# Performance work log

Hardware: AMD Instinct MI355X
Metric: run time of the kernel (lower is better)

Reference implementation:

```python
import jax, jax.numpy as jnp
import numpy as np
import math

N = 50000      # nodes
E = 800000     # edges
F_IN = 64      # input node features
H = 4          # heads
C = 32         # hidden_channels (per-head dim)
HC = H * C     # 128
ED = 4         # edge_dim
G = 1000       # graphs in batch


def _lin(key, fin, fout, bias=True):
    k1, k2 = jax.random.split(key)
    w = jax.random.normal(k1, (fin, fout), jnp.float32) * (1.0 / math.sqrt(fin))
    if bias:
        b = jax.random.normal(k2, (fout,), jnp.float32) * 0.02
        return w, b
    return w


def setup_inputs() -> dict:
    key = jax.random.key(0)
    ks = jax.random.split(key, 24)
    x = jax.random.normal(ks[0], (N, F_IN), jnp.float32)
    edge_index = jax.random.randint(ks[1], (2, E), 0, N)
    edge_attr = jax.random.normal(ks[2], (E, ED), jnp.float32)
    batch = jnp.sort(jax.random.randint(ks[3], (N,), 0, G))
    inp = {"x": x, "edge_index": edge_index, "edge_attr": edge_attr, "batch": batch}
    fins = [F_IN, HC, HC]
    i = 4
    for l in range(3):
        fin = fins[l]
        inp[f"wq{l+1}"], inp[f"bq{l+1}"] = _lin(ks[i], fin, HC); i += 1
        inp[f"wk{l+1}"], inp[f"bk{l+1}"] = _lin(ks[i], fin, HC); i += 1
        inp[f"wv{l+1}"], inp[f"bv{l+1}"] = _lin(ks[i], fin, HC); i += 1
        inp[f"we{l+1}"] = _lin(ks[i], ED, HC, bias=False); i += 1
        inp[f"ws{l+1}"], inp[f"bs{l+1}"] = _lin(ks[i], fin, HC); i += 1
    inp["wlin"], inp["blin"] = _lin(ks[i], HC, 1)
    return inp


def _segment_softmax(alpha, seg, n):
    # numerically-stable softmax over edges grouped by destination node
    m = jax.ops.segment_max(alpha, seg, num_segments=n)
    m = jnp.where(jnp.isfinite(m), m, 0.0)
    a = jnp.exp(alpha - m[seg])
    s = jax.ops.segment_sum(a, seg, num_segments=n)
    return a / (s[seg] + 1e-16)


def _conv(x, src, dst, ea, wq, bq, wk, bk, wv, bv, we, ws, bs):
    # PyG TransformerConv (concat=True, root_weight=True, beta=False)
    n = x.shape[0]
    q = (x @ wq + bq).reshape(n, H, C)
    k = (x @ wk + bk).reshape(n, H, C)
    v = (x @ wv + bv).reshape(n, H, C)
    e = (ea @ we).reshape(-1, H, C)          # [E,H,C] edge projection
    kj = k[src] + e                           # key of source + edge
    alpha = jnp.einsum('ehc,ehc->eh', q[dst], kj) / math.sqrt(C)  # [E,H]
    alpha = _segment_softmax(alpha, dst, n)
    msg = (v[src] + e) * alpha[..., None]     # [E,H,C]
    out = jax.ops.segment_sum(msg, dst, num_segments=n).reshape(n, HC)
    return out + x @ ws + bs                  # skip connection


def reference(x, edge_index, edge_attr, batch,
              wq1, bq1, wk1, bk1, wv1, bv1, we1, ws1, bs1,
              wq2, bq2, wk2, bk2, wv2, bv2, we2, ws2, bs2,
              wq3, bq3, wk3, bk3, wv3, bv3, we3, ws3, bs3,
              wlin, blin):
    src, dst = edge_index[0], edge_index[1]
    h = jax.nn.relu(_conv(x, src, dst, edge_attr, wq1, bq1, wk1, bk1, wv1, bv1, we1, ws1, bs1))
    h = jax.nn.relu(_conv(h, src, dst, edge_attr, wq2, bq2, wk2, bk2, wv2, bv2, we2, ws2, bs2))
    h = _conv(h, src, dst, edge_attr, wq3, bq3, wk3, bk3, wv3, bv3, we3, ws3, bs3)
    # global_mean_pool
    s = jax.ops.segment_sum(h, batch, num_segments=G)
    cnt = jax.ops.segment_sum(jnp.ones((h.shape[0],), h.dtype), batch, num_segments=G)
    pooled = s / jnp.maximum(cnt, 1.0)[:, None]
    # dropout is identity in eval mode
    return pooled @ wlin + blin
```

## Files before the change

kernel.cpp:

```cpp
#include <hip/hip_runtime.h>
#include <math.h>

#define NN 50000
#define EE 800000
#define GG 1000

typedef __attribute__((ext_vector_type(4))) _Float16 h4f;
typedef __attribute__((ext_vector_type(8))) _Float16 h8f;
typedef __attribute__((ext_vector_type(4))) float f32x4;

static inline int ceil_div(int a, int b) { return (a + b - 1) / b; }

union EU { int2 i; h4f h; };


__global__ __launch_bounds__(256) void hist_k(const int* __restrict__ ei, int* __restrict__ cnt)
{
    int e = blockIdx.x * 256 + threadIdx.x;
    if (e >= EE) return;
    atomicAdd(&cnt[ei[EE + e]], 1);
}

__global__ __launch_bounds__(1024) void scan1_k(const int* __restrict__ cnt, int n,
                                                int* __restrict__ rowptr, int* __restrict__ bsum)
{
    __shared__ int tmp[1024];
    const int tid = threadIdx.x;
    const int i = blockIdx.x * 1024 + tid;
    tmp[tid] = (i < n) ? cnt[i] : 0;
    __syncthreads();
    for (int off = 1; off < 1024; off <<= 1) {
        int t = (tid >= off) ? tmp[tid - off] : 0;
        __syncthreads();
        tmp[tid] += t;
        __syncthreads();
    }
    if (i < n) rowptr[i + 1] = tmp[tid];
    if (tid == 1023) bsum[blockIdx.x] = tmp[1023];
}

__global__ void scan2_k(int* __restrict__ bsum, int nb)
{
    if (threadIdx.x == 0) {
        int run = 0;
        for (int i = 0; i < nb; ++i) { int t = bsum[i]; bsum[i] = run; run += t; }
    }
}

__global__ __launch_bounds__(1024) void scan3_k(int* __restrict__ rowptr,
                                                int* __restrict__ wcur,
                                                const int* __restrict__ bsum, int n)
{
    int i = blockIdx.x * 1024 + threadIdx.x;
    if (i < n) {
        int v = rowptr[i + 1] + bsum[blockIdx.x];
        rowptr[i + 1] = v;
        if (i + 1 < n) wcur[i + 1] = v;
    }
    if (i == 0) { rowptr[0] = 0; wcur[0] = 0; }
}

__global__ __launch_bounds__(256) void scatter_k(const int* __restrict__ ei,
                                                 const float4* __restrict__ ea,
                                                 int* __restrict__ wcur,
                                                 int4* __restrict__ edges)
{
    int e = blockIdx.x * 256 + threadIdx.x;
    if (e >= EE) return;
    int dst = ei[EE + e];
    int pos = atomicAdd(&wcur[dst], 1);
    float4 a = ea[e];
    EU u; u.h = h4f{(_Float16)a.x, (_Float16)a.y, (_Float16)a.z, (_Float16)a.w};
    edges[pos] = make_int4(ei[e], u.i.x, u.i.y, 0);
}


__global__ __launch_bounds__(256) void cvt_h(const float* __restrict__ in,
                                             _Float16* __restrict__ out, int n4)
{
    int i = blockIdx.x * 256 + threadIdx.x;
    if (i >= n4) return;
    float4 v = reinterpret_cast<const float4*>(in)[i];
    h4f h = {(_Float16)v.x, (_Float16)v.y, (_Float16)v.z, (_Float16)v.w};
    reinterpret_cast<h4f*>(out)[i] = h;
}

struct W12 { const float* w[12]; };

__global__ __launch_bounds__(64) void shuffle_w12(W12 ws, _Float16* __restrict__ out)
{
    const int m = blockIdx.y;
    const int K = (m < 4) ? 64 : 128;
    const int nblk = (K / 16) * 8;
    if (blockIdx.x >= nblk) return;
    const int s = blockIdx.x >> 3, c16 = blockIdx.x & 7;
    const int lane = threadIdx.x;
    const float* __restrict__ w = ws.w[m];
    const int kbase = s * 16 + (lane >> 4) * 4;
    const int col = c16 * 16 + (lane & 15);
    h4f h;
#pragma unroll
    for (int j = 0; j < 4; ++j) h[j] = (_Float16)w[(size_t)(kbase + j) * 128 + col];
    size_t base = (m < 4) ? (size_t)m * 64 * 128
                          : (size_t)4 * 64 * 128 + (size_t)(m - 4) * 128 * 128;
    reinterpret_cast<h4f*>(out + base)[(size_t)blockIdx.x * 64 + lane] = h;
}

template<int K>
__global__ __launch_bounds__(256) void gemm_mfma(
    const _Float16* __restrict__ xh, const _Float16* __restrict__ wshuf,
    const float* __restrict__ bq, const float* __restrict__ bk,
    const float* __restrict__ bv, const float* __restrict__ bs,
    _Float16* __restrict__ qout, _Float16* __restrict__ kout,
    _Float16* __restrict__ vout, float* __restrict__ skout)
{
    constexpr int KS = K / 16;
    constexpr int PADK = K + 8;
    __shared__ _Float16 xs[64 * PADK];
    const int t = threadIdx.x;
    const int bn = blockIdx.x * 64;
    constexpr int CH = K / 8;
    for (int idx = t; idx < 64 * CH; idx += 256) {
        const int row = idx / CH, ch = idx % CH;
        h8f val = {0, 0, 0, 0, 0, 0, 0, 0};
        if (bn + row < NN)
            val = reinterpret_cast<const h8f*>(xh + (size_t)(bn + row) * K)[ch];
        *reinterpret_cast<h8f*>(&xs[row * PADK + ch * 8]) = val;
    }
    __syncthreads();

    const int wid = t >> 6, lane = t & 63;
    const int rloc = wid * 16 + (lane & 15);
    const int ko = (lane >> 4) * 4;
    h4f b[KS];
#pragma unroll
    for (int s = 0; s < KS; ++s)
        b[s] = *reinterpret_cast<const h4f*>(&xs[rloc * PADK + s * 16 + ko]);

    const int node = bn + rloc;
    const int hcq = (lane >> 4) * 4;
    const float* bias[4] = {bq, bk, bv, bs};

#pragma unroll
    for (int m = 0; m < 4; ++m) {
        const h4f* __restrict__ wm = reinterpret_cast<const h4f*>(wshuf + (size_t)m * K * 128);
        f32x4 acc[8];
#pragma unroll
        for (int c = 0; c < 8; ++c) acc[c] = {0, 0, 0, 0};
#pragma unroll
        for (int c = 0; c < 8; ++c)
#pragma unroll
            for (int s = 0; s < KS; ++s) {
                h4f af = wm[(s * 8 + c) * 64 + lane];
                acc[c] = __builtin_amdgcn_mfma_f32_16x16x16f16(af, b[s], acc[c], 0, 0, 0);
            }
        if (node < NN) {
            const float* bm = bias[m];
#pragma unroll
            for (int c = 0; c < 8; ++c) {
                const int hc = c * 16 + hcq;
                const float4 bb = *reinterpret_cast<const float4*>(&bm[hc]);
                float o0 = acc[c][0] + bb.x, o1 = acc[c][1] + bb.y;
                float o2 = acc[c][2] + bb.z, o3 = acc[c][3] + bb.w;
                if (m == 3) {
                    *reinterpret_cast<float4*>(&skout[(size_t)node * 128 + hc]) =
                        make_float4(o0, o1, o2, o3);
                } else {
                    _Float16* dst = (m == 0) ? qout : (m == 1) ? kout : vout;
                    h4f oh = {(_Float16)o0, (_Float16)o1, (_Float16)o2, (_Float16)o3};
                    *reinterpret_cast<h4f*>(&dst[(size_t)node * 128 + hc]) = oh;
                }
            }
        }
    }
}

__global__ __launch_bounds__(256) void node_agg(
    const int* __restrict__ rowptr, const int4* __restrict__ edges,
    const _Float16* __restrict__ qh, const _Float16* __restrict__ kh,
    const _Float16* __restrict__ vh, const float* __restrict__ we,
    const float* __restrict__ sk, _Float16* __restrict__ houth, int relu)
{
    __shared__ float4 we_s[128];
    const int t = threadIdx.x;
    if (t < 128) we_s[t] = reinterpret_cast<const float4*>(we)[t];
    __syncthreads();
    const int node = blockIdx.x * 8 + (t >> 5);
    if (node >= NN) return;
    const int lane = t & 31;
    const int beg = rowptr[node], end = rowptr[node + 1];

    const float4 w0 = we_s[lane], w1 = we_s[32 + lane], w2 = we_s[64 + lane], w3 = we_s[96 + lane];

    const h4f qv = *reinterpret_cast<const h4f*>(&qh[(size_t)node * 128 + lane * 4]);
    const float sc = 0.17677669529663687f;
    const float4 qf = make_float4((float)qv[0] * sc, (float)qv[1] * sc,
                                  (float)qv[2] * sc, (float)qv[3] * sc);

    float p0 = w0.x * qf.x + w0.y * qf.y + w0.z * qf.z + w0.w * qf.w;
    float p1 = w1.x * qf.x + w1.y * qf.y + w1.z * qf.z + w1.w * qf.w;
    float p2 = w2.x * qf.x + w2.y * qf.y + w2.z * qf.z + w2.w * qf.w;
    float p3 = w3.x * qf.x + w3.y * qf.y + w3.z * qf.z + w3.w * qf.w;
#pragma unroll
    for (int off = 1; off < 8; off <<= 1) {
        p0 += __shfl_xor(p0, off); p1 += __shfl_xor(p1, off);
        p2 += __shfl_xor(p2, off); p3 += __shfl_xor(p3, off);
    }
    const float qe0 = p0, qe1 = p1, qe2 = p2, qe3 = p3;

    float m = -INFINITY, s = 0.f;
    float4 acc = make_float4(0.f, 0.f, 0.f, 0.f);
    float T0 = 0.f, T1 = 0.f, T2 = 0.f, T3 = 0.f;

    int p = beg;
    for (; p + 1 < end; p += 2) {
        const int4 rA = edges[p], rB = edges[p + 1];
        EU uA, uB; uA.i = make_int2(rA.y, rA.z); uB.i = make_int2(rB.y, rB.z);
        const h4f eaA = uA.h, eaB = uB.h;
        const h4f kA = *reinterpret_cast<const h4f*>(&kh[(size_t)rA.x * 128 + lane * 4]);
        const h4f kB = *reinterpret_cast<const h4f*>(&kh[(size_t)rB.x * 128 + lane * 4]);
        const h4f vA = *reinterpret_cast<const h4f*>(&vh[(size_t)rA.x * 128 + lane * 4]);
        const h4f vB = *reinterpret_cast<const h4f*>(&vh[(size_t)rB.x * 128 + lane * 4]);
        float alA = qf.x * (float)kA[0] + qf.y * (float)kA[1]
                  + qf.z * (float)kA[2] + qf.w * (float)kA[3];
        float alB = qf.x * (float)kB[0] + qf.y * (float)kB[1]
                  + qf.z * (float)kB[2] + qf.w * (float)kB[3];
        alA += __shfl_xor(alA, 1); alA += __shfl_xor(alA, 2); alA += __shfl_xor(alA, 4);
        alB += __shfl_xor(alB, 1); alB += __shfl_xor(alB, 2); alB += __shfl_xor(alB, 4);
        const float fA0 = (float)eaA[0], fA1 = (float)eaA[1],
                    fA2 = (float)eaA[2], fA3 = (float)eaA[3];
        const float fB0 = (float)eaB[0], fB1 = (float)eaB[1],
                    fB2 = (float)eaB[2], fB3 = (float)eaB[3];
        alA += fA0 * qe0 + fA1 * qe1 + fA2 * qe2 + fA3 * qe3;
        alB += fB0 * qe0 + fB1 * qe1 + fB2 * qe2 + fB3 * qe3;
        const float mn = fmaxf(m, fmaxf(alA, alB));
        const float r  = __expf(m - mn);
        const float pA = __expf(alA - mn), pB = __expf(alB - mn);
        s = s * r + pA + pB;
        acc.x = acc.x * r + pA * (float)vA[0] + pB * (float)vB[0];
        acc.y = acc.y * r + pA * (float)vA[1] + pB * (float)vB[1];
        acc.z = acc.z * r + pA * (float)vA[2] + pB * (float)vB[2];
        acc.w = acc.w * r + pA * (float)vA[3] + pB * (float)vB[3];
        T0 = T0 * r + pA * fA0 + pB * fB0;
        T1 = T1 * r + pA * fA1 + pB * fB1;
        T2 = T2 * r + pA * fA2 + pB * fB2;
        T3 = T3 * r + pA * fA3 + pB * fB3;
        m = mn;
    }
    if (p < end) {
        const int4 rA = edges[p];
        EU uA; uA.i = make_int2(rA.y, rA.z);
        const h4f eaA = uA.h;
        const h4f kA = *reinterpret_cast<const h4f*>(&kh[(size_t)rA.x * 128 + lane * 4]);
        const h4f vA = *reinterpret_cast<const h4f*>(&vh[(size_t)rA.x * 128 + lane * 4]);
        float alA = qf.x * (float)kA[0] + qf.y * (float)kA[1]
                  + qf.z * (float)kA[2] + qf.w * (float)kA[3];
        alA += __shfl_xor(alA, 1); alA += __shfl_xor(alA, 2); alA += __shfl_xor(alA, 4);
        const float fA0 = (float)eaA[0], fA1 = (float)eaA[1],
                    fA2 = (float)eaA[2], fA3 = (float)eaA[3];
        alA += fA0 * qe0 + fA1 * qe1 + fA2 * qe2 + fA3 * qe3;
        const float mn = fmaxf(m, alA);
        const float r  = __expf(m - mn);
        const float pA = __expf(alA - mn);
        s = s * r + pA;
        acc.x = acc.x * r + pA * (float)vA[0];
        acc.y = acc.y * r + pA * (float)vA[1];
        acc.z = acc.z * r + pA * (float)vA[2];
        acc.w = acc.w * r + pA * (float)vA[3];
        T0 = T0 * r + pA * fA0;
        T1 = T1 * r + pA * fA1;
        T2 = T2 * r + pA * fA2;
        T3 = T3 * r + pA * fA3;
        m = mn;
    }
    const float inv = 1.0f / (s + 1e-16f);
    const float4 sk4 = *reinterpret_cast<const float4*>(&sk[(size_t)node * 128 + lane * 4]);
    float o0 = (acc.x + w0.x * T0 + w1.x * T1 + w2.x * T2 + w3.x * T3) * inv + sk4.x;
    float o1 = (acc.y + w0.y * T0 + w1.y * T1 + w2.y * T2 + w3.y * T3) * inv + sk4.y;
    float o2 = (acc.z + w0.z * T0 + w1.z * T1 + w2.z * T2 + w3.z * T3) * inv + sk4.z;
    float o3 = (acc.w + w0.w * T0 + w1.w * T1 + w2.w * T2 + w3.w * T3) * inv + sk4.w;
    if (relu) {
        o0 = fmaxf(o0, 0.f); o1 = fmaxf(o1, 0.f);
        o2 = fmaxf(o2, 0.f); o3 = fmaxf(o3, 0.f);
    }
    h4f oh = {(_Float16)o0, (_Float16)o1, (_Float16)o2, (_Float16)o3};
    *reinterpret_cast<h4f*>(&houth[(size_t)node * 128 + lane * 4]) = oh;
}


__global__ __launch_bounds__(256) void boundaries_k(const int* __restrict__ batch,
                                                    int* __restrict__ gptr)
{
    int i = blockIdx.x * 256 + threadIdx.x;
    if (i >= NN) return;
    int b = batch[i];
    int bp = (i == 0) ? -1 : batch[i - 1];
    for (int g = bp + 1; g <= b; ++g) gptr[g] = i;
    if (i == NN - 1) for (int g = b + 1; g <= GG; ++g) gptr[g] = NN;
}

__global__ __launch_bounds__(128) void head_k(
    const _Float16* __restrict__ h, const int* __restrict__ gptr,
    const float* __restrict__ wlin, const float* __restrict__ blin,
    float* __restrict__ out)
{
    __shared__ float red[128];
    const int g = blockIdx.x;
    const int t = threadIdx.x;
    const int beg = gptr[g], end = gptr[g + 1];
    float p = 0.f;
    for (int n = beg; n < end; ++n) p += (float)h[(size_t)n * 128 + t];
    p *= wlin[t];
    red[t] = p;
    __syncthreads();
    for (int off = 64; off; off >>= 1) {
        if (t < off) red[t] += red[t + off];
        __syncthreads();
    }
    if (t == 0) out[g] = red[0] / fmaxf((float)(end - beg), 1.0f) + blin[0];
}

extern "C" void kernel_launch(void* const* d_in, const int* in_sizes, int n_in,
                              void* d_out, int out_size, void* d_ws, size_t ws_size,
                              hipStream_t stream)
{
    const float* x     = (const float*)d_in[0];
    const int*   ei    = (const int*)d_in[1];
    const float* ea    = (const float*)d_in[2];
    const int*   batch = (const int*)d_in[3];
    auto W = [&](int i) { return (const float*)d_in[i]; };

    char* wsb = (char*)d_ws;
    size_t off = 0;
    auto alloc = [&](size_t bytes) { void* p = wsb + off; off += (bytes + 15) & ~15ull; return p; };

    float* sk       = (float*)alloc((size_t)NN * 128 * 4);
    int4*  edges    = (int4*)alloc((size_t)EE * 16);
    _Float16* qh    = (_Float16*)alloc((size_t)NN * 128 * 2);
    _Float16* kh    = (_Float16*)alloc((size_t)NN * 128 * 2);
    _Float16* vh    = (_Float16*)alloc((size_t)NN * 128 * 2);
    _Float16* hh    = (_Float16*)alloc((size_t)NN * 128 * 2);
    _Float16* wshuf = (_Float16*)alloc(((size_t)4 * 64 * 128 + 8 * 128 * 128) * 2);
    int* cnt    = (int*)alloc((size_t)NN * 4);
    int* rowptr = (int*)alloc((size_t)(NN + 1) * 4);
    int* wcur   = (int*)alloc((size_t)NN * 4);
    int* gptr   = (int*)alloc((size_t)(GG + 1) * 4);
    int* bsum   = (int*)alloc((size_t)64 * 4);

    hipMemsetAsync(cnt, 0, NN * sizeof(int), stream);
    hist_k<<<ceil_div(EE, 256), 256, 0, stream>>>(ei, cnt);
    const int NB = ceil_div(NN, 1024);
    scan1_k<<<NB, 1024, 0, stream>>>(cnt, NN, rowptr, bsum);
    scan2_k<<<1, 64, 0, stream>>>(bsum, NB);
    scan3_k<<<NB, 1024, 0, stream>>>(rowptr, wcur, bsum, NN);
    scatter_k<<<ceil_div(EE, 256), 256, 0, stream>>>(ei, (const float4*)ea, wcur, edges);

    cvt_h<<<ceil_div(NN * 64 / 4, 256), 256, 0, stream>>>(x, hh, NN * 64 / 4);
    boundaries_k<<<ceil_div(NN, 256), 256, 0, stream>>>(batch, gptr);

    W12 w12 = {{ W(4), W(6), W(8), W(11),
                 W(13), W(15), W(17), W(20),
                 W(22), W(24), W(26), W(29) }};
    shuffle_w12<<<dim3(64, 12), 64, 0, stream>>>(w12, wshuf);
    const size_t wsz1 = (size_t)4 * 64 * 128;
    const size_t wsz2 = (size_t)4 * 128 * 128;

    auto layer = [&](int K, const _Float16* wsh, int relu, int wb) {
        if (K == 64)
            gemm_mfma<64><<<ceil_div(NN, 64), 256, 0, stream>>>(
                hh, wsh, W(wb + 1), W(wb + 3), W(wb + 5), W(wb + 8), qh, kh, vh, sk);
        else
            gemm_mfma<128><<<ceil_div(NN, 64), 256, 0, stream>>>(
                hh, wsh, W(wb + 1), W(wb + 3), W(wb + 5), W(wb + 8), qh, kh, vh, sk);
        node_agg<<<ceil_div(NN, 8), 256, 0, stream>>>(
            rowptr, edges, qh, kh, vh, W(wb + 6), sk, hh, relu);
    };

    layer(64,  wshuf, 1, 4);
    layer(128, wshuf + wsz1, 1, 13);
    layer(128, wshuf + wsz1 + wsz2, 0, 22);

    head_k<<<GG, 128, 0, stream>>>(hh, gptr, W(31), W(32), (float*)d_out);
}
```

Baseline: 509.1 us.

## Fuse input fp16 conversion into GEMM, stage weights in LDS, unroll edge loop

Several changes at once. The standalone fp32-to-fp16 conversion kernel is removed and the first-layer GEMM converts x while loading it. Each GEMM block now copies its weight matrix into shared memory before the MFMA loop, which adds block-wide barriers and LDS use (up to 32KB extra). The node aggregation loop is unrolled from 2 to 4 edges per iteration and uses exp2f with the log2(e) factor folded into the query scale. The serial block-sum scan is replaced with a wavefront shuffle scan.

```diff
diff --git a/kernel.cpp b/kernel.cpp
--- a/kernel.cpp
+++ b/kernel.cpp
@@ -39,12 +39,16 @@
     if (tid == 1023) bsum[blockIdx.x] = tmp[1023];
 }
 
-__global__ void scan2_k(int* __restrict__ bsum, int nb)
-{
-    if (threadIdx.x == 0) {
-        int run = 0;
-        for (int i = 0; i < nb; ++i) { int t = bsum[i]; bsum[i] = run; run += t; }
-    }
+__global__ __launch_bounds__(64) void scan2_k(int* __restrict__ bsum, int nb)
+{
+    const int t = threadIdx.x;
+    int v = (t < nb) ? bsum[t] : 0;
+    const int orig = v;
+    for (int off = 1; off < 64; off <<= 1) {
+        int n = __shfl_up(v, off);
+        if (t >= off) v += n;
+    }
+    if (t < nb) bsum[t] = v - orig;
 }
 
 __global__ __launch_bounds__(1024) void scan3_k(int* __restrict__ rowptr,
@@ -72,17 +76,6 @@
     float4 a = ea[e];
     EU u; u.h = h4f{(_Float16)a.x, (_Float16)a.y, (_Float16)a.z, (_Float16)a.w};
     edges[pos] = make_int4(ei[e], u.i.x, u.i.y, 0);
-}
-
-
-__global__ __launch_bounds__(256) void cvt_h(const float* __restrict__ in,
-                                             _Float16* __restrict__ out, int n4)
-{
-    int i = blockIdx.x * 256 + threadIdx.x;
-    if (i >= n4) return;
-    float4 v = reinterpret_cast<const float4*>(in)[i];
-    h4f h = {(_Float16)v.x, (_Float16)v.y, (_Float16)v.z, (_Float16)v.w};
-    reinterpret_cast<h4f*>(out)[i] = h;
 }
 
 struct W12 { const float* w[12]; };
@@ -106,9 +99,9 @@
     reinterpret_cast<h4f*>(out + base)[(size_t)blockIdx.x * 64 + lane] = h;
 }
 
-template<int K>
+template<int K, bool F32IN>
 __global__ __launch_bounds__(256) void gemm_mfma(
-    const _Float16* __restrict__ xh, const _Float16* __restrict__ wshuf,
+    const void* __restrict__ xin, const _Float16* __restrict__ wshuf,
     const float* __restrict__ bq, const float* __restrict__ bk,
     const float* __restrict__ bv, const float* __restrict__ bs,
     _Float16* __restrict__ qout, _Float16* __restrict__ kout,
@@ -117,15 +110,30 @@
     constexpr int KS = K / 16;
     constexpr int PADK = K + 8;
     __shared__ _Float16 xs[64 * PADK];
+    __shared__ _Float16 wt[K * 128];
     const int t = threadIdx.x;
     const int bn = blockIdx.x * 64;
-    constexpr int CH = K / 8;
-    for (int idx = t; idx < 64 * CH; idx += 256) {
-        const int row = idx / CH, ch = idx % CH;
-        h8f val = {0, 0, 0, 0, 0, 0, 0, 0};
-        if (bn + row < NN)
-            val = reinterpret_cast<const h8f*>(xh + (size_t)(bn + row) * K)[ch];
-        *reinterpret_cast<h8f*>(&xs[row * PADK + ch * 8]) = val;
+    if (F32IN) {
+        const float* xf = (const float*)xin;
+        constexpr int C4 = K / 4;
+        for (int idx = t; idx < 64 * C4; idx += 256) {
+            const int row = idx / C4, c4 = idx % C4;
+            float4 val = make_float4(0.f, 0.f, 0.f, 0.f);
+            if (bn + row < NN)
+                val = reinterpret_cast<const float4*>(xf)[(size_t)(bn + row) * C4 + c4];
+            h4f h = {(_Float16)val.x, (_Float16)val.y, (_Float16)val.z, (_Float16)val.w};
+            *reinterpret_cast<h4f*>(&xs[row * PADK + c4 * 4]) = h;
+        }
+    } else {
+        const _Float16* xh = (const _Float16*)xin;
+        constexpr int CH = K / 8;
+        for (int idx = t; idx < 64 * CH; idx += 256) {
+            const int row = idx / CH, ch = idx % CH;
+            h8f val = {0, 0, 0, 0, 0, 0, 0, 0};
+            if (bn + row < NN)
+                val = reinterpret_cast<const h8f*>(xh + (size_t)(bn + row) * K)[ch];
+            *reinterpret_cast<h8f*>(&xs[row * PADK + ch * 8]) = val;
+        }
     }
     __syncthreads();
 
@@ -140,10 +148,15 @@
     const int node = bn + rloc;
     const int hcq = (lane >> 4) * 4;
     const float* bias[4] = {bq, bk, bv, bs};
+    constexpr int WH4 = K * 128 / 4;
 
 #pragma unroll
     for (int m = 0; m < 4; ++m) {
-        const h4f* __restrict__ wm = reinterpret_cast<const h4f*>(wshuf + (size_t)m * K * 128);
+        const h4f* __restrict__ wg = reinterpret_cast<const h4f*>(wshuf + (size_t)m * K * 128);
+        h4f* __restrict__ wl = reinterpret_cast<h4f*>(wt);
+        for (int idx = t; idx < WH4; idx += 256) wl[idx] = wg[idx];
+        __syncthreads();
+
         f32x4 acc[8];
 #pragma unroll
         for (int c = 0; c < 8; ++c) acc[c] = {0, 0, 0, 0};
@@ -151,7 +164,7 @@
         for (int c = 0; c < 8; ++c)
 #pragma unroll
             for (int s = 0; s < KS; ++s) {
-                h4f af = wm[(s * 8 + c) * 64 + lane];
+                h4f af = wl[(s * 8 + c) * 64 + lane];
                 acc[c] = __builtin_amdgcn_mfma_f32_16x16x16f16(af, b[s], acc[c], 0, 0, 0);
             }
         if (node < NN) {
@@ -172,6 +185,7 @@
                 }
             }
         }
+        __syncthreads();
     }
 }
 
@@ -193,7 +207,7 @@
     const float4 w0 = we_s[lane], w1 = we_s[32 + lane], w2 = we_s[64 + lane], w3 = we_s[96 + lane];
 
     const h4f qv = *reinterpret_cast<const h4f*>(&qh[(size_t)node * 128 + lane * 4]);
-    const float sc = 0.17677669529663687f;
+    const float sc = 0.17677669529663687f * 1.4426950408889634f;
     const float4 qf = make_float4((float)qv[0] * sc, (float)qv[1] * sc,
                                   (float)qv[2] * sc, (float)qv[3] * sc);
 
@@ -213,55 +227,76 @@
     float T0 = 0.f, T1 = 0.f, T2 = 0.f, T3 = 0.f;
 
     int p = beg;
-    for (; p + 1 < end; p += 2) {
-        const int4 rA = edges[p], rB = edges[p + 1];
-        EU uA, uB; uA.i = make_int2(rA.y, rA.z); uB.i = make_int2(rB.y, rB.z);
-        const h4f eaA = uA.h, eaB = uB.h;
+    for (; p + 3 < end; p += 4) {
+        const int4 rA = edges[p], rB = edges[p + 1], rC = edges[p + 2], rD = edges[p + 3];
+        EU uA, uB, uC, uD;
+        uA.i = make_int2(rA.y, rA.z); uB.i = make_int2(rB.y, rB.z);
+        uC.i = make_int2(rC.y, rC.z); uD.i = make_int2(rD.y, rD.z);
         const h4f kA = *reinterpret_cast<const h4f*>(&kh[(size_t)rA.x * 128 + lane * 4]);
         const h4f kB = *reinterpret_cast<const h4f*>(&kh[(size_t)rB.x * 128 + lane * 4]);
+        const h4f kC = *reinterpret_cast<const h4f*>(&kh[(size_t)rC.x * 128 + lane * 4]);
+        const h4f kD = *reinterpret_cast<const h4f*>(&kh[(size_t)rD.x * 128 + lane * 4]);
         const h4f vA = *reinterpret_cast<const h4f*>(&vh[(size_t)rA.x * 128 + lane * 4]);
         const h4f vB = *reinterpret_cast<const h4f*>(&vh[(size_t)rB.x * 128 + lane * 4]);
+        const h4f vC = *reinterpret_cast<const h4f*>(&vh[(size_t)rC.x * 128 + lane * 4]);
+        const h4f vD = *reinterpret_cast<const h4f*>(&vh[(size_t)rD.x * 128 + lane * 4]);
         float alA = qf.x * (float)kA[0] + qf.y * (float)kA[1]
                   + qf.z * (float)kA[2] + qf.w * (float)kA[3];
         float alB = qf.x * (float)kB[0] + qf.y * (float)kB[1]
                   + qf.z * (float)kB[2] + qf.w * (float)kB[3];
+        float alC = qf.x * (float)kC[0] + qf.y * (float)kC[1]
+                  + qf.z * (float)kC[2] + qf.w * (float)kC[3];
+        float alD = qf.x * (float)kD[0] + qf.y * (float)kD[1]
+                  + qf.z * (float)kD[2] + qf.w * (float)kD[3];
         alA += __shfl_xor(alA, 1); alA += __shfl_xor(alA, 2); alA += __shfl_xor(alA, 4);
         alB += __shfl_xor(alB, 1); alB += __shfl_xor(alB, 2); alB += __shfl_xor(alB, 4);
-        const float fA0 = (float)eaA[0], fA1 = (float)eaA[1],
-                    fA2 = (float)eaA[2], fA3 = (float)eaA[3];
-        const float fB0 = (float)eaB[0], fB1 = (float)eaB[1],
-                    fB2 = (float)eaB[2], fB3 = (float)eaB[3];
+        alC += __shfl_xor(alC, 1); alC += __shfl_xor(alC, 2); alC += __shfl_xor(alC, 4);
+        alD += __shfl_xor(alD, 1); alD += __shfl_xor(alD, 2); alD += __shfl_xor(alD, 4);
+        const float fA0 = (float)uA.h[0], fA1 = (float)uA.h[1],
+                    fA2 = (float)uA.h[2], fA3 = (float)uA.h[3];
+        const float fB0 = (float)uB.h[0], fB1 = (float)uB.h[1],
+                    fB2 = (float)uB.h[2], fB3 = (float)uB.h[3];
+        const float fC0 = (float)uC.h[0], fC1 = (float)uC.h[1],
+                    fC2 = (float)uC.h[2], fC3 = (float)uC.h[3];
+        const float fD0 = (float)uD.h[0], fD1 = (float)uD.h[1],
+                    fD2 = (float)uD.h[2], fD3 = (float)uD.h[3];
         alA += fA0 * qe0 + fA1 * qe1 + fA2 * qe2 + fA3 * qe3;
         alB += fB0 * qe0 + fB1 * qe1 + fB2 * qe2 + fB3 * qe3;
-        const float mn = fmaxf(m, fmaxf(alA, alB));
-        const float r  = __expf(m - mn);
-        const float pA = __expf(alA - mn), pB = __expf(alB - mn);
-        s = s * r + pA + pB;
-        acc.x = acc.x * r + pA * (float)vA[0] + pB * (float)vB[0];
-        acc.y = acc.y * r + pA * (float)vA[1] + pB * (float)vB[1];
-        acc.z = acc.z * r + pA * (float)vA[2] + pB * (float)vB[2];
-        acc.w = acc.w * r + pA * (float)vA[3] + pB * (float)vB[3];
-        T0 = T0 * r + pA * fA0 + pB * fB0;
-        T1 = T1 * r + pA * fA1 + pB * fB1;
-        T2 = T2 * r + pA * fA2 + pB * fB2;
-        T3 = T3 * r + pA * fA3 + pB * fB3;
+        alC += fC0 * qe0 + fC1 * qe1 + fC2 * qe2 + fC3 * qe3;
+        alD += fD0 * qe0 + fD1 * qe1 + fD2 * qe2 + fD3 * qe3;
+        const float mn = fmaxf(fmaxf(fmaxf(alA, alB), fmaxf(alC, alD)), m);
+        const float r  = exp2f(m - mn);
+        const float pA = exp2f(alA - mn), pB = exp2f(alB - mn);
+        const float pC = exp2f(alC - mn), pD = exp2f(alD - mn);
+        s = s * r + pA + pB + pC + pD;
+        acc.x = acc.x * r + pA * (float)vA[0] + pB * (float)vB[0]
+                          + pC * (float)vC[0] + pD * (float)vD[0];
+        acc.y = acc.y * r + pA * (float)vA[1] + pB * (float)vB[1]
+                          + pC * (float)vC[1] + pD * (float)vD[1];
+        acc.z = acc.z * r + pA * (float)vA[2] + pB * (float)vB[2]
+                          + pC * (float)vC[2] + pD * (float)vD[2];
+        acc.w = acc.w * r + pA * (float)vA[3] + pB * (float)vB[3]
+                          + pC * (float)vC[3] + pD * (float)vD[3];
+        T0 = T0 * r + pA * fA0 + pB * fB0 + pC * fC0 + pD * fD0;
+        T1 = T1 * r + pA * fA1 + pB * fB1 + pC * fC1 + pD * fD1;
+        T2 = T2 * r + pA * fA2 + pB * fB2 + pC * fC2 + pD * fD2;
+        T3 = T3 * r + pA * fA3 + pB * fB3 + pC * fC3 + pD * fD3;
         m = mn;
     }
-    if (p < end) {
+    for (; p < end; ++p) {
         const int4 rA = edges[p];
         EU uA; uA.i = make_int2(rA.y, rA.z);
-        const h4f eaA = uA.h;
         const h4f kA = *reinterpret_cast<const h4f*>(&kh[(size_t)rA.x * 128 + lane * 4]);
         const h4f vA = *reinterpret_cast<const h4f*>(&vh[(size_t)rA.x * 128 + lane * 4]);
         float alA = qf.x * (float)kA[0] + qf.y * (float)kA[1]
                   + qf.z * (float)kA[2] + qf.w * (float)kA[3];
         alA += __shfl_xor(alA, 1); alA += __shfl_xor(alA, 2); alA += __shfl_xor(alA, 4);
-        const float fA0 = (float)eaA[0], fA1 = (float)eaA[1],
-                    fA2 = (float)eaA[2], fA3 = (float)eaA[3];
+        const float fA0 = (float)uA.h[0], fA1 = (float)uA.h[1],
+                    fA2 = (float)uA.h[2], fA3 = (float)uA.h[3];
         alA += fA0 * qe0 + fA1 * qe1 + fA2 * qe2 + fA3 * qe3;
         const float mn = fmaxf(m, alA);
-        const float r  = __expf(m - mn);
-        const float pA = __expf(alA - mn);
+        const float r  = exp2f(m - mn);
+        const float pA = exp2f(alA - mn);
         s = s * r + pA;
         acc.x = acc.x * r + pA * (float)vA[0];
         acc.y = acc.y * r + pA * (float)vA[1];
@@ -355,7 +390,6 @@
     scan3_k<<<NB, 1024, 0, stream>>>(rowptr, wcur, bsum, NN);
     scatter_k<<<ceil_div(EE, 256), 256, 0, stream>>>(ei, (const float4*)ea, wcur, edges);
 
-    cvt_h<<<ceil_div(NN * 64 / 4, 256), 256, 0, stream>>>(x, hh, NN * 64 / 4);
     boundaries_k<<<ceil_div(NN, 256), 256, 0, stream>>>(batch, gptr);
 
     W12 w12 = {{ W(4), W(6), W(8), W(11),
@@ -365,20 +399,20 @@
     const size_t wsz1 = (size_t)4 * 64 * 128;
     const size_t wsz2 = (size_t)4 * 128 * 128;
 
-    auto layer = [&](int K, const _Float16* wsh, int relu, int wb) {
+    auto layer = [&](int K, const void* xin, const _Float16* wsh, int relu, int wb) {
         if (K == 64)
-            gemm_mfma<64><<<ceil_div(NN, 64), 256, 0, stream>>>(
-                hh, wsh, W(wb + 1), W(wb + 3), W(wb + 5), W(wb + 8), qh, kh, vh, sk);
+            gemm_mfma<64, true><<<ceil_div(NN, 64), 256, 0, stream>>>(
+                xin, wsh, W(wb + 1), W(wb + 3), W(wb + 5), W(wb + 8), qh, kh, vh, sk);
         else
-            gemm_mfma<128><<<ceil_div(NN, 64), 256, 0, stream>>>(
-                hh, wsh, W(wb + 1), W(wb + 3), W(wb + 5), W(wb + 8), qh, kh, vh, sk);
+            gemm_mfma<128, false><<<ceil_div(NN, 64), 256, 0, stream>>>(
+                xin, wsh, W(wb + 1), W(wb + 3), W(wb + 5), W(wb + 8), qh, kh, vh, sk);
         node_agg<<<ceil_div(NN, 8), 256, 0, stream>>>(
             rowptr, edges, qh, kh, vh, W(wb + 6), sk, hh, relu);
     };
 
-    layer(64,  wshuf, 1, 4);
-    layer(128, wshuf + wsz1, 1, 13);
-    layer(128, wshuf + wsz1 + wsz2, 0, 22);
+    layer(64,  x,  wshuf, 1, 4);
+    layer(128, hh, wshuf + wsz1, 1, 13);
+    layer(128, hh, wshuf + wsz1 + wsz2, 0, 22);
 
     head_k<<<GG, 128, 0, stream>>>(hh, gptr, W(31), W(32), (float*)d_out);
 }
```

Measured after the change: 495.0 us. -2.8%, faster.
